# Kernel optimization log

Hardware: AMD Instinct MI355X
Metric: run time of the kernel (lower is better)

Reference implementation:

```python
import jax, jax.numpy as jnp
import numpy as np

EMBED_DIM = 1024
NUM_HEADS = 16
HEAD_DIM = EMBED_DIM // NUM_HEADS
SCALE = HEAD_DIM ** -0.5


def setup_inputs() -> dict:
    key = jax.random.key(0)
    ks = jax.random.split(key, 12)
    B, S, D = 4, 2048, EMBED_DIM
    x = jax.random.normal(ks[0], (B, S, D), dtype=jnp.float32)
    key_padding_mask = jax.random.randint(ks[1], (B, S), 0, 2).astype(jnp.bool_)
    init = 1.0 / np.sqrt(D)
    def lin(kw, kb):
        W = jax.random.uniform(kw, (D, D), minval=-init, maxval=init, dtype=jnp.float32)
        b = jax.random.uniform(kb, (D,), minval=-init, maxval=init, dtype=jnp.float32)
        return W, b
    Wq, bq = lin(ks[2], ks[3])
    Wk, bk = lin(ks[4], ks[5])
    Wv, bv = lin(ks[6], ks[7])
    Wo, bo = lin(ks[8], ks[9])
    return {"x": x, "key_padding_mask": key_padding_mask,
            "Wq": Wq, "bq": bq, "Wk": Wk, "bk": bk,
            "Wv": Wv, "bv": bv, "Wo": Wo, "bo": bo}


def reference(x, key_padding_mask, Wq, bq, Wk, bk, Wv, bv, Wo, bo):
    B, S, D = x.shape
    H, Hd = NUM_HEADS, HEAD_DIM
    # projections (torch Linear: y = x @ W.T + b)
    q = (x @ Wq.T + bq).reshape(B, S, H, Hd).transpose(0, 2, 1, 3)  # [B,H,S,Hd]
    k = (x @ Wk.T + bk).reshape(B, S, H, Hd).transpose(0, 2, 1, 3)
    v = (x @ Wv.T + bv).reshape(B, S, H, Hd).transpose(0, 2, 1, 3)
    scores = jnp.einsum('bhqd,bhkd->bhqk', q, k) * SCALE  # [B,H,S,S]
    mask = key_padding_mask[:, None, None, :]  # [B,1,1,S]
    scores = jnp.where(mask, -jnp.inf, scores)
    probs = jax.nn.softmax(scores, axis=-1)
    # dropout p=0.0 (inference) -> identity
    out = jnp.einsum('bhqk,bhkd->bhqd', probs, v)  # [B,H,S,Hd]
    out = out.transpose(0, 2, 1, 3).reshape(B, S, D)
    return out @ Wo.T + bo
```

## Files before the change

### kernel.cpp

```cpp
#include <hip/hip_runtime.h>
#include <stdint.h>

typedef __bf16 bf16;
typedef __bf16 bf16x8 __attribute__((ext_vector_type(8)));
typedef float f32x4 __attribute__((ext_vector_type(4)));

#define SEQ 2048
#define NHEAD 16
#define HDIM 64
#define DMODEL 1024
#define NBATCH 4
#define ATT_SCALE 0.18033688011112042f
#define SEQHD (SEQ * HDIM)
#define BHSTRIDE (2 * SEQHD)


__device__ __forceinline__ void gload_lds16(const bf16* g, bf16* l) {
  __builtin_amdgcn_global_load_lds(
      (const __attribute__((address_space(1))) uint32_t*)g,
      (__attribute__((address_space(3))) uint32_t*)l, 16, 0, 0);
}

__device__ __forceinline__ uint32_t pk2(float a, float b) {
  bf16 x = (bf16)a, y = (bf16)b;
  return (uint32_t)__builtin_bit_cast(uint16_t, x) |
         ((uint32_t)__builtin_bit_cast(uint16_t, y) << 16);
}

__global__ __launch_bounds__(256) void cvt_kernel(const float* __restrict__ src,
                                                  bf16* __restrict__ dst) {
  size_t i = ((size_t)blockIdx.x * 256 + threadIdx.x) * 16;
#pragma unroll
  for (int j = 0; j < 2; ++j) {
    float4 f0 = *(const float4*)(src + i + j * 8);
    float4 f1 = *(const float4*)(src + i + j * 8 + 4);
    bf16x8 v;
    v[0] = (bf16)f0.x; v[1] = (bf16)f0.y; v[2] = (bf16)f0.z; v[3] = (bf16)f0.w;
    v[4] = (bf16)f1.x; v[5] = (bf16)f1.y; v[6] = (bf16)f1.z; v[7] = (bf16)f1.w;
    *(bf16x8*)(dst + i + j * 8) = v;
  }
}

__global__ __launch_bounds__(256) void prep_kernel(
    const float* __restrict__ Wq, const float* __restrict__ Wk,
    const float* __restrict__ Wv, bf16* __restrict__ Wbf3,
    int* __restrict__ posv, int* __restrict__ inv) {
  __shared__ int sums[256];
  const int bx = blockIdx.x, t = threadIdx.x;
  if (bx < 768) {
    const float* s = bx < 256 ? Wq : (bx < 512 ? Wk : Wv);
    bf16* d = Wbf3 + (size_t)(bx >> 8) * DMODEL * DMODEL;
    size_t i = ((size_t)(bx & 255) * 256 + t) * 16;
#pragma unroll
    for (int j = 0; j < 2; ++j) {
      float4 f0 = *(const float4*)(s + i + j * 8);
      float4 f1 = *(const float4*)(s + i + j * 8 + 4);
      bf16x8 v;
      v[0] = (bf16)f0.x; v[1] = (bf16)f0.y; v[2] = (bf16)f0.z; v[3] = (bf16)f0.w;
      v[4] = (bf16)f1.x; v[5] = (bf16)f1.y; v[6] = (bf16)f1.z; v[7] = (bf16)f1.w;
      *(bf16x8*)(d + i + j * 8) = v;
    }
    return;
  }
  const int b = bx - 768;
  int* m = posv + b * SEQ;
  int* iv = inv + b * SEQ;
  int f[8], cnt = 0;
#pragma unroll
  for (int j = 0; j < 8; ++j) {
    int x = m[t * 8 + j];
    int unm = (x < 0) ? 0 : ((x & 0x40000000) ? 1 : (x == 0 ? 1 : 0));
    f[j] = unm; cnt += unm;
    iv[t * 8 + j] = 0;
  }
  sums[t] = cnt;
  __syncthreads();
  if (t == 0) {
    int acc = 0;
#pragma unroll 8
    for (int i = 0; i < 256; ++i) { int s = sums[i]; sums[i] = acc; acc += s; }
  }
  __syncthreads();
  int p = sums[t];
#pragma unroll
  for (int j = 0; j < 8; ++j) {
    m[t * 8 + j] = (int)((f[j] ? 0x40000000u : 0x80000000u) | (unsigned)p);
    if (f[j]) iv[p] = t * 8 + j;
    p += f[j];
  }
}

__global__ __launch_bounds__(256) void qproj_kernel(
    const bf16* __restrict__ xb, const bf16* __restrict__ Wall,
    const float* __restrict__ bq, bf16* __restrict__ Qall) {
  __shared__ __align__(16) bf16 lW[64 * 64];
  __shared__ __align__(16) bf16 lXw[4][32 * 64];
  const int t = threadIdx.x, wave = t >> 6, lane = t & 63;
  const int quad = lane >> 4, c = lane & 15;
  const int m0 = blockIdx.x * 128;
  const int h = blockIdx.y;
  const bf16* W = Wall + (size_t)(h * HDIM) * DMODEL;
  bf16* pw = lXw[wave];
  const int sr = lane >> 3, sg = lane & 7;
  const bf16* aS = xb + (size_t)(m0 + wave * 32 + sr) * DMODEL + ((sg ^ sr) * 8);
  const bf16* wS = W + (size_t)(wave * 8 + sr) * DMODEL + ((sg ^ sr) * 8);
  f32x4 acc[2][4] = {};
  for (int k0 = 0; k0 < DMODEL; k0 += 64) {
    __syncthreads();
    gload_lds16(wS + k0, lW + wave * 512);
    gload_lds16(wS + 32 * DMODEL + k0, lW + wave * 512 + 2048);
#pragma unroll
    for (int ii = 0; ii < 4; ++ii)
      gload_lds16(aS + k0 + (size_t)ii * 8 * DMODEL, pw + ii * 512);
    __syncthreads();
#pragma unroll
    for (int kk = 0; kk < 2; ++kk) {
      bf16x8 af[2], bfr[4];
#pragma unroll
      for (int mi = 0; mi < 2; ++mi) {
        int row = mi * 16 + c;
        af[mi] = *(const bf16x8*)(pw + row * 64 + (((kk * 4 + quad) ^ (row & 7)) * 8));
      }
#pragma unroll
      for (int ni = 0; ni < 4; ++ni) {
        int row = ni * 16 + c;
        bfr[ni] = *(const bf16x8*)(lW + row * 64 + (((kk * 4 + quad) ^ (row & 7)) * 8));
      }
#pragma unroll
      for (int mi = 0; mi < 2; ++mi)
#pragma unroll
        for (int ni = 0; ni < 4; ++ni)
          acc[mi][ni] = __builtin_amdgcn_mfma_f32_16x16x32_bf16(af[mi], bfr[ni], acc[mi][ni], 0, 0, 0);
    }
  }
#pragma unroll
  for (int ni = 0; ni < 4; ++ni) {
    int hd = ni * 16 + c;
    float bqv = bq[h * HDIM + hd];
#pragma unroll
    for (int mi = 0; mi < 2; ++mi)
#pragma unroll
      for (int r = 0; r < 4; ++r) {
        int tok = m0 + wave * 32 + mi * 16 + quad * 4 + r;
        int b = tok >> 11, s = tok & 2047;
        Qall[((size_t)(b * NHEAD + h) * SEQ + s) * HDIM + hd] =
            (bf16)((acc[mi][ni][r] + bqv) * ATT_SCALE);
      }
  }
}

__global__ __launch_bounds__(256) void kvproj_kernel(
    const bf16* __restrict__ xb, const bf16* __restrict__ Wall,
    const float* __restrict__ bk, const float* __restrict__ bv,
    const int* __restrict__ posv, const int* __restrict__ inv,
    bf16* __restrict__ kv) {
  __shared__ __align__(16) bf16 lW[64 * 64];
  __shared__ __align__(16) bf16 lXw[4][32 * 64];
  const int t = threadIdx.x, wave = t >> 6, lane = t & 63;
  const int quad = lane >> 4, c = lane & 15;
  const int bx = blockIdx.x;
  const int b_loc = bx >> 4, mb = bx & 15;
  const int nt = blockIdx.y;
  const int isV = nt >> 4, h = nt & 15;
  int v2 = posv[b_loc * SEQ + SEQ - 1];
  int nk = (v2 & 0x3FFFFFFF) + (v2 >= 0 ? 1 : 0);
  const int c0 = mb * 128;
  if (c0 >= nk) return;
  const bf16* W = Wall + (size_t)(1 + isV) * DMODEL * DMODEL + (size_t)(h * HDIM) * DMODEL;
  const float* bias = (isV ? bv : bk) + h * HDIM;
  bf16* pw = lXw[wave];
  const int sr = lane >> 3, sg = lane & 7;
  const int swzc = (sg ^ sr) * 8;
  const bf16* wS = W + (size_t)(wave * 8 + sr) * DMODEL + swzc;
  const int* invb = inv + b_loc * SEQ;
  int grow[4];
#pragma unroll
  for (int ii = 0; ii < 4; ++ii)
    grow[ii] = invb[c0 + wave * 32 + ii * 8 + sr];
  const bf16* xbb = xb + (size_t)b_loc * SEQ * DMODEL + swzc;
  f32x4 acc[2][4] = {};
  for (int k0 = 0; k0 < DMODEL; k0 += 64) {
    __syncthreads();
    gload_lds16(wS + k0, lW + wave * 512);
    gload_lds16(wS + 32 * DMODEL + k0, lW + wave * 512 + 2048);
#pragma unroll
    for (int ii = 0; ii < 4; ++ii)
      gload_lds16(xbb + (size_t)grow[ii] * DMODEL + k0, pw + ii * 512);
    __syncthreads();
#pragma unroll
    for (int kk = 0; kk < 2; ++kk) {
      bf16x8 af[2], bfr[4];
#pragma unroll
      for (int mi = 0; mi < 2; ++mi) {
        int row = mi * 16 + c;
        af[mi] = *(const bf16x8*)(pw + row * 64 + (((kk * 4 + quad) ^ (row & 7)) * 8));
      }
#pragma unroll
      for (int ni = 0; ni < 4; ++ni) {
        int row = ni * 16 + c;
        bfr[ni] = *(const bf16x8*)(lW + row * 64 + (((kk * 4 + quad) ^ (row & 7)) * 8));
      }
#pragma unroll
      for (int mi = 0; mi < 2; ++mi)
#pragma unroll
        for (int ni = 0; ni < 4; ++ni)
          acc[mi][ni] = __builtin_amdgcn_mfma_f32_16x16x32_bf16(af[mi], bfr[ni], acc[mi][ni], 0, 0, 0);
    }
  }
  bf16* base = kv + (size_t)(b_loc * NHEAD + h) * BHSTRIDE;
#pragma unroll
  for (int ni = 0; ni < 4; ++ni) {
    int hd = ni * 16 + c;
    float bv_ = bias[hd];
#pragma unroll
    for (int mi = 0; mi < 2; ++mi)
#pragma unroll
      for (int r = 0; r < 4; ++r) {
        int dst = c0 + wave * 32 + mi * 16 + quad * 4 + r;
        float val = (dst < nk) ? (acc[mi][ni][r] + bv_) : 0.0f;
        if (isV) base[SEQHD + (size_t)hd * SEQ + dst] = (bf16)val;
        else     base[(size_t)dst * HDIM + hd] = (bf16)val;
      }
  }
}

__global__ __launch_bounds__(256, 4) void attn4_kernel(
    const bf16* __restrict__ Qall, const bf16* __restrict__ KV,
    const int* __restrict__ posv, bf16* __restrict__ O, int chunk) {
  __shared__ __align__(16) bf16 lK[2][64 * 64];
  __shared__ __align__(16) bf16 lV[2][64 * 64];
  __shared__ __align__(16) bf16 lPw[4][16 * 64];
  const int t = threadIdx.x, wave = t >> 6, lane = t & 63;
  const int quad = lane >> 4, c = lane & 15;
  const int i = blockIdx.x;
  const int xcd = i & 7, slot = i >> 3;
  const int bhl = xcd * 4 + (slot >> 5);
  const int qt = slot & 31;
  const int b_loc = bhl >> 4, h = bhl & 15;
  const int b = chunk * 2 + b_loc;
  const int q0 = qt * 64 + wave * 16;
  const bf16* Qh = Qall + (size_t)(b * NHEAD + h) * SEQHD;
  const bf16* Kb = KV + (size_t)(b_loc * NHEAD + h) * BHSTRIDE;
  const bf16* Vtb = Kb + SEQHD;
  bf16* pw = lPw[wave];

  int v2 = posv[b * SEQ + SEQ - 1];
  int nk = (v2 & 0x3FFFFFFF) + (v2 >= 0 ? 1 : 0);
  int NT = ((nk + 63) >> 6) << 6;

  const int srow = t >> 3;
  const int sswz = (t & 7) ^ (srow & 7);
  const bf16* kSrc = Kb + (size_t)srow * HDIM + sswz * 8;
  const bf16* vSrc = Vtb + (size_t)srow * SEQ + sswz * 8;
  const int sOff = wave * 512;

  bf16x8 qf[2];
#pragma unroll
  for (int kk = 0; kk < 2; ++kk)
    qf[kk] = *(const bf16x8*)(Qh + (size_t)(q0 + c) * HDIM + kk * 32 + quad * 8);

  f32x4 oacc[4] = {};
  float mrun = -1e30f, lrun = 0.0f;

  const int pbase = c * 64 + (quad & 1) * 4;
  const int pswz = c & 7;

#pragma unroll
  for (int i2 = 0; i2 < 2; ++i2) {
    gload_lds16(kSrc + i2 * 32 * HDIM, &lK[0][0] + sOff + i2 * 2048);
    gload_lds16(vSrc + (size_t)i2 * 32 * SEQ, &lV[0][0] + sOff + i2 * 2048);
  }
  __syncthreads();

  int idx = 0;
  for (int kt = 0; kt < NT; kt += 64, idx ^= 1) {
    if (kt + 64 < NT) {
      const bf16* ks = kSrc + (size_t)(kt + 64) * HDIM;
      const bf16* vs = vSrc + (kt + 64);
      bf16* kD = &lK[0][0] + (idx ^ 1) * 4096 + sOff;
      bf16* vD = &lV[0][0] + (idx ^ 1) * 4096 + sOff;
#pragma unroll
      for (int i2 = 0; i2 < 2; ++i2) {
        gload_lds16(ks + i2 * 32 * HDIM, kD + i2 * 2048);
        gload_lds16(vs + (size_t)i2 * 32 * SEQ, vD + i2 * 2048);
      }
    }
    const bf16* lKc = &lK[0][0] + idx * 4096;
    const bf16* lVc = &lV[0][0] + idx * 4096;

    f32x4 sacc[4] = {};
#pragma unroll
    for (int kk = 0; kk < 2; ++kk) {
      bf16x8 kf[4];
#pragma unroll
      for (int ni = 0; ni < 4; ++ni) {
        int row = ni * 16 + c;
        kf[ni] = *(const bf16x8*)(lKc + row * 64 + (((kk * 4 + quad) ^ (row & 7)) * 8));
      }
#pragma unroll
      for (int ni = 0; ni < 4; ++ni)
        sacc[ni] = __builtin_amdgcn_mfma_f32_16x16x32_bf16(kf[ni], qf[kk], sacc[ni], 0, 0, 0);
    }

    if (kt + 64 > nk) {
      int base = kt + quad * 4 - nk;
#pragma unroll
      for (int ni = 0; ni < 4; ++ni)
#pragma unroll
        for (int r = 0; r < 4; ++r)
          if (base + ni * 16 + r >= 0) sacc[ni][r] = -3e38f;
    }

    float m1 = fmaxf(fmaxf(sacc[0][0], sacc[0][1]), sacc[0][2]);
    float m2 = fmaxf(fmaxf(sacc[0][3], sacc[1][0]), sacc[1][1]);
    float m3 = fmaxf(fmaxf(sacc[1][2], sacc[1][3]), sacc[2][0]);
    float m4 = fmaxf(fmaxf(sacc[2][1], sacc[2][2]), sacc[2][3]);
    float m5 = fmaxf(fmaxf(sacc[3][0], sacc[3][1]), sacc[3][2]);
    float mx = fmaxf(fmaxf(fmaxf(m1, m2), m3), fmaxf(fmaxf(m4, m5), sacc[3][3]));
    mx = fmaxf(mx, __shfl_xor(mx, 16));
    mx = fmaxf(mx, __shfl_xor(mx, 32));

    if (!__all(mx - mrun <= 8.0f)) {
      float mn = fmaxf(mrun, mx);
      float al = __builtin_amdgcn_exp2f(mrun - mn);
      mrun = mn;
      lrun *= al;
      float al4[4];
#pragma unroll
      for (int r = 0; r < 4; ++r) al4[r] = __shfl(al, quad * 4 + r);
#pragma unroll
      for (int ni = 0; ni < 4; ++ni)
#pragma unroll
        for (int r = 0; r < 4; ++r) oacc[ni][r] *= al4[r];
    }

    float rs = 0.0f;
#pragma unroll
    for (int ni = 0; ni < 4; ++ni)
#pragma unroll
      for (int r = 0; r < 4; ++r) {
        float e = __builtin_amdgcn_exp2f(sacc[ni][r] - mrun);
        sacc[ni][r] = e; rs += e;
      }
    rs += __shfl_xor(rs, 16);
    rs += __shfl_xor(rs, 32);
    lrun += rs;

#pragma unroll
    for (int ni = 0; ni < 4; ++ni) {
      uint2 u;
      u.x = pk2(sacc[ni][0], sacc[ni][1]);
      u.y = pk2(sacc[ni][2], sacc[ni][3]);
      int sl = pbase + (((ni * 2 + (quad >> 1)) ^ pswz) * 8);
      *(uint2*)(pw + sl) = u;
    }

#pragma unroll
    for (int kk = 0; kk < 2; ++kk) {
      bf16x8 pf, vfr[4];
      pf = *(const bf16x8*)(pw + c * 64 + (((kk * 4 + quad) ^ (c & 7)) * 8));
#pragma unroll
      for (int ni = 0; ni < 4; ++ni) {
        int row = ni * 16 + c;
        vfr[ni] = *(const bf16x8*)(lVc + row * 64 + (((kk * 4 + quad) ^ (row & 7)) * 8));
      }
#pragma unroll
      for (int ni = 0; ni < 4; ++ni)
        oacc[ni] = __builtin_amdgcn_mfma_f32_16x16x32_bf16(pf, vfr[ni], oacc[ni], 0, 0, 0);
    }

    __syncthreads();
  }

  float linv = lrun > 0.0f ? 1.0f / lrun : 0.0f;
  float linv4[4];
#pragma unroll
  for (int r = 0; r < 4; ++r) linv4[r] = __shfl(linv, quad * 4 + r);
#pragma unroll
  for (int r = 0; r < 4; ++r) {
    size_t tok = (size_t)b * SEQ + q0 + quad * 4 + r;
#pragma unroll
    for (int ni = 0; ni < 4; ++ni)
      O[tok * DMODEL + h * HDIM + ni * 16 + c] = (bf16)(oacc[ni][r] * linv4[r]);
  }
}

__global__ __launch_bounds__(256) void outproj_kernel(
    const bf16* __restrict__ O, const bf16* __restrict__ Wob,
    const float* __restrict__ bo, float* __restrict__ out) {
  __shared__ __align__(16) bf16 lW[64 * 64];
  __shared__ __align__(16) bf16 lXw[4][32 * 64];
  const int t = threadIdx.x, wave = t >> 6, lane = t & 63;
  const int quad = lane >> 4, c = lane & 15;
  const int m0 = blockIdx.x * 128;
  const int n0 = blockIdx.y * 64;
  bf16* pw = lXw[wave];
  const int sr = lane >> 3, sg = lane & 7;
  const bf16* aS = O + (size_t)(m0 + wave * 32 + sr) * DMODEL + ((sg ^ sr) * 8);
  const bf16* wS = Wob + (size_t)(n0 + wave * 8 + sr) * DMODEL + ((sg ^ sr) * 8);
  f32x4 acc[2][4] = {};
  for (int k0 = 0; k0 < DMODEL; k0 += 64) {
    __syncthreads();
    gload_lds16(wS + k0, lW + wave * 512);
    gload_lds16(wS + 32 * DMODEL + k0, lW + wave * 512 + 2048);
#pragma unroll
    for (int ii = 0; ii < 4; ++ii)
      gload_lds16(aS + k0 + (size_t)ii * 8 * DMODEL, pw + ii * 512);
    __syncthreads();
#pragma unroll
    for (int kk = 0; kk < 2; ++kk) {
      bf16x8 af[2], bfr[4];
#pragma unroll
      for (int mi = 0; mi < 2; ++mi) {
        int row = mi * 16 + c;
        af[mi] = *(const bf16x8*)(pw + row * 64 + (((kk * 4 + quad) ^ (row & 7)) * 8));
      }
#pragma unroll
      for (int ni = 0; ni < 4; ++ni) {
        int row = ni * 16 + c;
        bfr[ni] = *(const bf16x8*)(lW + row * 64 + (((kk * 4 + quad) ^ (row & 7)) * 8));
      }
#pragma unroll
      for (int mi = 0; mi < 2; ++mi)
#pragma unroll
        for (int ni = 0; ni < 4; ++ni)
          acc[mi][ni] = __builtin_amdgcn_mfma_f32_16x16x32_bf16(af[mi], bfr[ni], acc[mi][ni], 0, 0, 0);
    }
  }
#pragma unroll
  for (int ni = 0; ni < 4; ++ni) {
    int gn = n0 + ni * 16 + c;
    float bv_ = bo[gn];
#pragma unroll
    for (int mi = 0; mi < 2; ++mi)
#pragma unroll
      for (int r = 0; r < 4; ++r) {
        int gm = m0 + wave * 32 + mi * 16 + quad * 4 + r;
        out[(size_t)gm * DMODEL + gn] = acc[mi][ni][r] + bv_;
      }
  }
}

extern "C" void kernel_launch(void* const* d_in, const int* in_sizes, int n_in,
                              void* d_out, int out_size, void* d_ws, size_t ws_size,
                              hipStream_t stream) {
  const float* x  = (const float*)d_in[0];
  int*         posv = (int*)d_in[1];
  const float* Wq = (const float*)d_in[2]; const float* bq = (const float*)d_in[3];
  const float* Wk = (const float*)d_in[4]; const float* bk = (const float*)d_in[5];
  const float* Wv = (const float*)d_in[6]; const float* bv = (const float*)d_in[7];
  const float* Wo = (const float*)d_in[8]; const float* bo = (const float*)d_in[9];
  float* out = (float*)d_out;
  char* outc = (char*)d_out;
  char* xc   = (char*)d_in[0];
  const size_t half = (size_t)NBATCH * SEQ * DMODEL * 2;
  const size_t qtr  = half / 2;

  bf16* Qall = (bf16*)d_out;
  bf16* xbf  = (bf16*)(outc + half);
  bf16* KV   = (bf16*)xc;
  bf16* O    = (bf16*)(xc + half);
  bf16* Wbf3 = (bf16*)(xc + half + qtr);
  int*  inv  = (int*)(xc + half + qtr + (size_t)3 * DMODEL * DMODEL * 2);
  bf16* Wobf = (bf16*)xc;

  cvt_kernel<<<dim3(2048), 256, 0, stream>>>(x, xbf);
  prep_kernel<<<dim3(772), 256, 0, stream>>>(Wq, Wk, Wv, Wbf3, posv, inv);
  qproj_kernel<<<dim3(64, 16), 256, 0, stream>>>(xbf, Wbf3, bq, Qall);
  kvproj_kernel<<<dim3(32, 32), 256, 0, stream>>>(xbf, Wbf3, bk, bv, posv, inv, KV);
  attn4_kernel<<<dim3(1024), 256, 0, stream>>>(Qall, KV, posv, O, 0);
  kvproj_kernel<<<dim3(32, 32), 256, 0, stream>>>(xbf + (size_t)2 * SEQ * DMODEL, Wbf3, bk, bv,
                                                  posv + 2 * SEQ, inv + 2 * SEQ, KV);
  attn4_kernel<<<dim3(1024), 256, 0, stream>>>(Qall, KV, posv, O, 1);
  cvt_kernel<<<dim3(256), 256, 0, stream>>>(Wo, Wobf);
  outproj_kernel<<<dim3(64, 16), 256, 0, stream>>>(O, Wobf, bo, out);
}
```

Before: 287.8 us.

## Merge Q, first KV projection and Wo conversion into one launch; add setprio

Replaces the separate Q-projection kernel, first KV-projection kernel and the Wo fp32-to-bf16 conversion with one kernel whose block index selects the role. The aim is to cut launch gaps and tail effects by letting these independent jobs share a single grid. Wobf now lives in the Wq input buffer, which is no longer needed after prep. The attention kernel also raises wave priority around its MFMA sections so matrix work gets scheduled ahead of other waves. The risks are overwriting an input buffer and uneven block cost inside the merged grid.

```diff
diff --git a/kernel.cpp b/kernel.cpp
--- a/kernel.cpp
+++ b/kernel.cpp
@@ -90,20 +90,106 @@
   }
 }
 
-__global__ __launch_bounds__(256) void qproj_kernel(
+__global__ __launch_bounds__(256) void mega_kernel(
     const bf16* __restrict__ xb, const bf16* __restrict__ Wall,
-    const float* __restrict__ bq, bf16* __restrict__ Qall) {
+    const float* __restrict__ bq, const float* __restrict__ bk,
+    const float* __restrict__ bv, const int* __restrict__ posv,
+    const int* __restrict__ inv, bf16* __restrict__ Qall,
+    bf16* __restrict__ kv, const float* __restrict__ Wo,
+    bf16* __restrict__ Wobf) {
   __shared__ __align__(16) bf16 lW[64 * 64];
   __shared__ __align__(16) bf16 lXw[4][32 * 64];
+  const int bx = blockIdx.x;
   const int t = threadIdx.x, wave = t >> 6, lane = t & 63;
   const int quad = lane >> 4, c = lane & 15;
-  const int m0 = blockIdx.x * 128;
-  const int h = blockIdx.y;
-  const bf16* W = Wall + (size_t)(h * HDIM) * DMODEL;
+  const int sr = lane >> 3, sg = lane & 7;
+  const int swzc = (sg ^ sr) * 8;
+
+  if (bx >= 2048) {
+    size_t i = ((size_t)(bx - 2048) * 256 + t) * 16;
+#pragma unroll
+    for (int j = 0; j < 2; ++j) {
+      float4 f0 = *(const float4*)(Wo + i + j * 8);
+      float4 f1 = *(const float4*)(Wo + i + j * 8 + 4);
+      bf16x8 v;
+      v[0] = (bf16)f0.x; v[1] = (bf16)f0.y; v[2] = (bf16)f0.z; v[3] = (bf16)f0.w;
+      v[4] = (bf16)f1.x; v[5] = (bf16)f1.y; v[6] = (bf16)f1.z; v[7] = (bf16)f1.w;
+      *(bf16x8*)(Wobf + i + j * 8) = v;
+    }
+    return;
+  }
+
+  if (bx < 1024) {
+    const int m0 = (bx & 63) * 128;
+    const int h = bx >> 6;
+    const bf16* W = Wall + (size_t)(h * HDIM) * DMODEL;
+    bf16* pw = lXw[wave];
+    const bf16* aS = xb + (size_t)(m0 + wave * 32 + sr) * DMODEL + swzc;
+    const bf16* wS = W + (size_t)(wave * 8 + sr) * DMODEL + swzc;
+    f32x4 acc[2][4] = {};
+    for (int k0 = 0; k0 < DMODEL; k0 += 64) {
+      __syncthreads();
+      gload_lds16(wS + k0, lW + wave * 512);
+      gload_lds16(wS + 32 * DMODEL + k0, lW + wave * 512 + 2048);
+#pragma unroll
+      for (int ii = 0; ii < 4; ++ii)
+        gload_lds16(aS + k0 + (size_t)ii * 8 * DMODEL, pw + ii * 512);
+      __syncthreads();
+#pragma unroll
+      for (int kk = 0; kk < 2; ++kk) {
+        bf16x8 af[2], bfr[4];
+#pragma unroll
+        for (int mi = 0; mi < 2; ++mi) {
+          int row = mi * 16 + c;
+          af[mi] = *(const bf16x8*)(pw + row * 64 + (((kk * 4 + quad) ^ (row & 7)) * 8));
+        }
+#pragma unroll
+        for (int ni = 0; ni < 4; ++ni) {
+          int row = ni * 16 + c;
+          bfr[ni] = *(const bf16x8*)(lW + row * 64 + (((kk * 4 + quad) ^ (row & 7)) * 8));
+        }
+#pragma unroll
+        for (int mi = 0; mi < 2; ++mi)
+#pragma unroll
+          for (int ni = 0; ni < 4; ++ni)
+            acc[mi][ni] = __builtin_amdgcn_mfma_f32_16x16x32_bf16(af[mi], bfr[ni], acc[mi][ni], 0, 0, 0);
+      }
+    }
+#pragma unroll
+    for (int ni = 0; ni < 4; ++ni) {
+      int hd = ni * 16 + c;
+      float bqv = bq[h * HDIM + hd];
+#pragma unroll
+      for (int mi = 0; mi < 2; ++mi)
+#pragma unroll
+        for (int r = 0; r < 4; ++r) {
+          int tok = m0 + wave * 32 + mi * 16 + quad * 4 + r;
+          int b = tok >> 11, s = tok & 2047;
+          Qall[((size_t)(b * NHEAD + h) * SEQ + s) * HDIM + hd] =
+              (bf16)((acc[mi][ni][r] + bqv) * ATT_SCALE);
+        }
+    }
+    return;
+  }
+
+  const int idx = bx - 1024;
+  const int xi = idx & 31, yi = idx >> 5;
+  const int b_loc = xi >> 4, mb = xi & 15;
+  const int isV = yi >> 4, h = yi & 15;
+  int v2 = posv[b_loc * SEQ + SEQ - 1];
+  int nk = (v2 & 0x3FFFFFFF) + (v2 >= 0 ? 1 : 0);
+  const int c0 = mb * 128;
+  if (c0 >= nk) return;
+  const bf16* W = Wall + (size_t)(1 + isV) * DMODEL * DMODEL + (size_t)(h * HDIM) * DMODEL;
+  const float* bias = (isV ? bv : bk) + h * HDIM;
   bf16* pw = lXw[wave];
-  const int sr = lane >> 3, sg = lane & 7;
-  const bf16* aS = xb + (size_t)(m0 + wave * 32 + sr) * DMODEL + ((sg ^ sr) * 8);
-  const bf16* wS = W + (size_t)(wave * 8 + sr) * DMODEL + ((sg ^ sr) * 8);
+  const bf16* wS = W + (size_t)(wave * 8 + sr) * DMODEL + swzc;
+  const int* invb = inv + b_loc * SEQ;
+  int grow[4];
+#pragma unroll
+  for (int ii = 0; ii < 4; ++ii)
+    grow[ii] = invb[c0 + wave * 32 + ii * 8 + sr];
+  const bf16* xbb = xb + (size_t)b_loc * SEQ * DMODEL + swzc;
   f32x4 acc[2][4] = {};
   for (int k0 = 0; k0 < DMODEL; k0 += 64) {
     __syncthreads();
@@ -111,7 +197,7 @@
     gload_lds16(wS + 32 * DMODEL + k0, lW + wave * 512 + 2048);
 #pragma unroll
     for (int ii = 0; ii < 4; ++ii)
-      gload_lds16(aS + k0 + (size_t)ii * 8 * DMODEL, pw + ii * 512);
+      gload_lds16(xbb + (size_t)grow[ii] * DMODEL + k0, pw + ii * 512);
     __syncthreads();
 #pragma unroll
     for (int kk = 0; kk < 2; ++kk) {
@@ -133,18 +219,19 @@
           acc[mi][ni] = __builtin_amdgcn_mfma_f32_16x16x32_bf16(af[mi], bfr[ni], acc[mi][ni], 0, 0, 0);
     }
   }
+  bf16* base = kv + (size_t)(b_loc * NHEAD + h) * BHSTRIDE;
 #pragma unroll
   for (int ni = 0; ni < 4; ++ni) {
     int hd = ni * 16 + c;
-    float bqv = bq[h * HDIM + hd];
+    float bv_ = bias[hd];
 #pragma unroll
     for (int mi = 0; mi < 2; ++mi)
 #pragma unroll
       for (int r = 0; r < 4; ++r) {
-        int tok = m0 + wave * 32 + mi * 16 + quad * 4 + r;
-        int b = tok >> 11, s = tok & 2047;
-        Qall[((size_t)(b * NHEAD + h) * SEQ + s) * HDIM + hd] =
-            (bf16)((acc[mi][ni][r] + bqv) * ATT_SCALE);
+        int dst = c0 + wave * 32 + mi * 16 + quad * 4 + r;
+        float val = (dst < nk) ? (acc[mi][ni][r] + bv_) : 0.0f;
+        if (isV) base[SEQHD + (size_t)hd * SEQ + dst] = (bf16)val;
+        else     base[(size_t)dst * HDIM + hd] = (bf16)val;
       }
   }
 }
@@ -289,6 +376,7 @@
     const bf16* lVc = &lV[0][0] + idx * 4096;
 
     f32x4 sacc[4] = {};
+    __builtin_amdgcn_s_setprio(1);
 #pragma unroll
     for (int kk = 0; kk < 2; ++kk) {
       bf16x8 kf[4];
@@ -301,6 +389,7 @@
       for (int ni = 0; ni < 4; ++ni)
         sacc[ni] = __builtin_amdgcn_mfma_f32_16x16x32_bf16(kf[ni], qf[kk], sacc[ni], 0, 0, 0);
     }
+    __builtin_amdgcn_s_setprio(0);
 
     if (kt + 64 > nk) {
       int base = kt + quad * 4 - nk;
@@ -355,6 +444,7 @@
       *(uint2*)(pw + sl) = u;
     }
 
+    __builtin_amdgcn_s_setprio(1);
 #pragma unroll
     for (int kk = 0; kk < 2; ++kk) {
       bf16x8 pf, vfr[4];
@@ -368,6 +458,7 @@
       for (int ni = 0; ni < 4; ++ni)
         oacc[ni] = __builtin_amdgcn_mfma_f32_16x16x32_bf16(pf, vfr[ni], oacc[ni], 0, 0, 0);
     }
+    __builtin_amdgcn_s_setprio(0);
 
     __syncthreads();
   }
@@ -462,16 +553,15 @@
   bf16* O    = (bf16*)(xc + half);
   bf16* Wbf3 = (bf16*)(xc + half + qtr);
   int*  inv  = (int*)(xc + half + qtr + (size_t)3 * DMODEL * DMODEL * 2);
-  bf16* Wobf = (bf16*)xc;
+  bf16* Wobf = (bf16*)d_in[2];
 
   cvt_kernel<<<dim3(2048), 256, 0, stream>>>(x, xbf);
   prep_kernel<<<dim3(772), 256, 0, stream>>>(Wq, Wk, Wv, Wbf3, posv, inv);
-  qproj_kernel<<<dim3(64, 16), 256, 0, stream>>>(xbf, Wbf3, bq, Qall);
-  kvproj_kernel<<<dim3(32, 32), 256, 0, stream>>>(xbf, Wbf3, bk, bv, posv, inv, KV);
+  mega_kernel<<<dim3(2304), 256, 0, stream>>>(xbf, Wbf3, bq, bk, bv, posv, inv,
+                                              Qall, KV, Wo, Wobf);
   attn4_kernel<<<dim3(1024), 256, 0, stream>>>(Qall, KV, posv, O, 0);
   kvproj_kernel<<<dim3(32, 32), 256, 0, stream>>>(xbf + (size_t)2 * SEQ * DMODEL, Wbf3, bk, bv,
                                                   posv + 2 * SEQ, inv + 2 * SEQ, KV);
   attn4_kernel<<<dim3(1024), 256, 0, stream>>>(Qall, KV, posv, O, 1);
-  cvt_kernel<<<dim3(256), 256, 0, stream>>>(Wo, Wobf);
   outproj_kernel<<<dim3(64, 16), 256, 0, stream>>>(O, Wobf, bo, out);
 }
```

Measured after the change: 274.9 us (median of 2 runs). 1.05x faster.
